# Kernel optimization log

Hardware: AMD Instinct MI355X
Metric: run time of the kernel (lower is better)

## Reference

```python
import jax, jax.numpy as jnp
import numpy as np

N_NODES = 50000
N_EDGES = 800000
D_IN = 128
D_OUT = 128
ALPHA = 0.2  # LeakyReLU negative slope


def setup_inputs() -> dict:
    key = jax.random.key(0)
    k1, k2, k3, k4 = jax.random.split(key, 4)
    x = jax.random.normal(k1, (N_NODES, D_IN), dtype=jnp.float32)
    W = jax.random.normal(k2, (D_IN, D_OUT), dtype=jnp.float32) * (1.414 / np.sqrt(D_IN))
    a = jax.random.normal(k3, (2 * D_OUT, 1), dtype=jnp.float32) * 0.1
    edge_index = jax.random.randint(k4, (2, N_EDGES), 0, N_NODES, dtype=jnp.int64)
    return {"x": x, "W": W, "a": a, "edge_index": edge_index}


def reference(x, W, a, edge_index):
    # h: (N, D_OUT)
    h = x @ W
    src, dst = edge_index[0], edge_index[1]
    # e_i = leakyrelu([h[src]; h[dst]] @ a) == leakyrelu((h@a1)[src] + (h@a2)[dst])
    a1 = a[:D_OUT, 0]
    a2 = a[D_OUT:, 0]
    s1 = h @ a1  # (N,)
    s2 = h @ a2  # (N,)
    e = jax.nn.leaky_relu(s1[src] + s2[dst], negative_slope=ALPHA)  # (E,)
    # Global softmax over all edges (faithful to F.softmax(edge_e, dim=0))
    attention = jax.nn.softmax(e)  # (E,)
    # output[dst] += attention * h[src]  (scatter-add)
    msgs = attention[:, None] * h[src]  # (E, D_OUT)
    output = jax.ops.segment_sum(msgs, dst, num_segments=N_NODES)
    return output
```

## Files before the change

### kernel.cpp

```cpp
#include <hip/hip_runtime.h>
#include <hip/hip_bf16.h>

#define N_NODES 50000
#define N_EDGES 800000
#define D 128
#define ALPHA 0.2f

#define KB_BLOCKS 3125
#define LDS_STRIDE 272

#define SCAN_PER 52
#define SCAN_PAD (1024 * SCAN_PER)

typedef __attribute__((ext_vector_type(8))) short short8;
typedef __attribute__((ext_vector_type(4))) float floatx4;

__device__ __forceinline__ unsigned int f2bf(float v)
{
    __hip_bfloat16 b = __float2bfloat16(v);
    return (unsigned int)*reinterpret_cast<unsigned short*>(&b);
}
__device__ __forceinline__ float bf_lo(unsigned int u)
{
    return __uint_as_float(u << 16);
}
__device__ __forceinline__ float bf_hi(unsigned int u)
{
    return __uint_as_float(u & 0xFFFF0000u);
}

__global__ __launch_bounds__(1024) void k_prep(
    const float* __restrict__ W, const float* __restrict__ a,
    float* __restrict__ w12, unsigned short* __restrict__ wb,
    int* __restrict__ deg, float* __restrict__ Z)
{
    const int t = threadIdx.x;
    const int b = blockIdx.x;
    deg[b * 1024 + t] = 0;
    if (b == 20 && t == 0) Z[0] = 0.f;

    if (b < 4) {
        const int g = b * 64 + (t >> 4);
        const int c = t & 15;
        const int which = g >> 7;
        const int r = g & 127;
        const float* wp = W + (size_t)r * D + c * 8;
        const float* ap = a + which * D + c * 8;
        const float4 u0 = *(const float4*)(wp);
        const float4 u1 = *(const float4*)(wp + 4);
        const float4 c0 = *(const float4*)(ap);
        const float4 c1 = *(const float4*)(ap + 4);
        float p = u0.x * c0.x + u0.y * c0.y + u0.z * c0.z + u0.w * c0.w
                + u1.x * c1.x + u1.y * c1.y + u1.z * c1.z + u1.w * c1.w;
        #pragma unroll
        for (int mask = 8; mask >= 1; mask >>= 1)
            p += __shfl_xor(p, mask);
        if (c == 0) w12[which * D + r] = p;
    } else if (b < 20) {
        const int f = (b - 4) * 1024 + t;
        const int j    = f & 7;
        const int lane = (f >> 3) & 63;
        const int half = (f >> 9) & 1;
        const int kt   = (f >> 10) & 3;
        const int wv   = f >> 12;
        const int q    = lane >> 4;
        const int nIdx = lane & 15;
        const float val =
            W[(size_t)(kt * 32 + q * 8 + j) * D + wv * 32 + 2 * nIdx + half];
        wb[f] = (unsigned short)f2bf(val);
    }
}

__global__ __launch_bounds__(256) void k_fused(
    const float* __restrict__ x, const float* __restrict__ w12,
    const unsigned short* __restrict__ wb, const int* __restrict__ ei,
    unsigned short* __restrict__ hb, float* __restrict__ s1,
    float* __restrict__ s2, int* __restrict__ deg, int* __restrict__ rank)
{
    __shared__ unsigned char lds[16 * LDS_STRIDE];
    const int t = threadIdx.x;
    const int rowbase = blockIdx.x * 16;

    const int r = t >> 4;
    const int c = t & 15;
    const float* xp = x + (size_t)(rowbase + r) * D + c * 8;
    const float4 v0 = *(const float4*)(xp);
    const float4 v1 = *(const float4*)(xp + 4);

    const int lane = t & 63;
    const int wv = t >> 6;
    const int q = lane >> 4;
    const int nIdx = lane & 15;
    const int n0 = wv * 32;
    const short8* wbp = (const short8*)wb;
    short8 B[2][4];
    #pragma unroll
    for (int kt = 0; kt < 4; ++kt) {
        B[0][kt] = wbp[((wv * 4 + kt) * 2 + 0) * 64 + lane];
        B[1][kt] = wbp[((wv * 4 + kt) * 2 + 1) * 64 + lane];
    }

    {
        const float* w1 = w12 + c * 8;
        const float* w2 = w12 + D + c * 8;
        float p1 = v0.x * w1[0] + v0.y * w1[1] + v0.z * w1[2] + v0.w * w1[3]
                 + v1.x * w1[4] + v1.y * w1[5] + v1.z * w1[6] + v1.w * w1[7];
        float p2 = v0.x * w2[0] + v0.y * w2[1] + v0.z * w2[2] + v0.w * w2[3]
                 + v1.x * w2[4] + v1.y * w2[5] + v1.z * w2[6] + v1.w * w2[7];
        #pragma unroll
        for (int mask = 8; mask >= 1; mask >>= 1) {
            p1 += __shfl_xor(p1, mask);
            p2 += __shfl_xor(p2, mask);
        }
        if (c == 0) { s1[rowbase + r] = p1; s2[rowbase + r] = p2; }

        uint4 pk;
        pk.x = f2bf(v0.x) | (f2bf(v0.y) << 16);
        pk.y = f2bf(v0.z) | (f2bf(v0.w) << 16);
        pk.z = f2bf(v1.x) | (f2bf(v1.y) << 16);
        pk.w = f2bf(v1.z) | (f2bf(v1.w) << 16);
        *(uint4*)(lds + r * LDS_STRIDE + c * 16) = pk;
    }
    __syncthreads();

    const unsigned char* ab = lds + nIdx * LDS_STRIDE + q * 16;
    const short8 A0 = *(const short8*)(ab);
    const short8 A1 = *(const short8*)(ab + 64);
    const short8 A2 = *(const short8*)(ab + 128);
    const short8 A3 = *(const short8*)(ab + 192);

    floatx4 acc0 = {0.f, 0.f, 0.f, 0.f};
    floatx4 acc1 = {0.f, 0.f, 0.f, 0.f};
    acc0 = __builtin_amdgcn_mfma_f32_16x16x32_bf16(A0, B[0][0], acc0, 0, 0, 0);
    acc1 = __builtin_amdgcn_mfma_f32_16x16x32_bf16(A0, B[1][0], acc1, 0, 0, 0);
    acc0 = __builtin_amdgcn_mfma_f32_16x16x32_bf16(A1, B[0][1], acc0, 0, 0, 0);
    acc1 = __builtin_amdgcn_mfma_f32_16x16x32_bf16(A1, B[1][1], acc1, 0, 0, 0);
    acc0 = __builtin_amdgcn_mfma_f32_16x16x32_bf16(A2, B[0][2], acc0, 0, 0, 0);
    acc1 = __builtin_amdgcn_mfma_f32_16x16x32_bf16(A2, B[1][2], acc1, 0, 0, 0);
    acc0 = __builtin_amdgcn_mfma_f32_16x16x32_bf16(A3, B[0][3], acc0, 0, 0, 0);
    acc1 = __builtin_amdgcn_mfma_f32_16x16x32_bf16(A3, B[1][3], acc1, 0, 0, 0);

    #pragma unroll
    for (int i = 0; i < 4; ++i) {
        const int row = rowbase + q * 4 + i;
        const unsigned int pk = f2bf(acc0[i]) | (f2bf(acc1[i]) << 16);
        *(unsigned int*)(hb + (size_t)row * D + n0 + 2 * nIdx) = pk;
    }

    const int e = blockIdx.x * 256 + t;
    rank[e] = atomicAdd(&deg[ei[N_EDGES + e]], 1);
}

__global__ __launch_bounds__(1024) void k_scan(
    const int* __restrict__ deg, int* __restrict__ offs)
{
    const int t = threadIdx.x;
    const int lane = t & 63;
    const int wv = t >> 6;
    __shared__ int wsum[16];
    const int base = t * SCAN_PER;
    int4 v[13];
    const int4* dp = (const int4*)(deg + base);
    int s = 0;
    #pragma unroll
    for (int k = 0; k < 13; ++k) {
        v[k] = dp[k];
        s += v[k].x + v[k].y + v[k].z + v[k].w;
    }
    int inc = s;
    #pragma unroll
    for (int off = 1; off < 64; off <<= 1) {
        int u = __shfl_up(inc, off);
        if (lane >= off) inc += u;
    }
    if (lane == 63) wsum[wv] = inc;
    __syncthreads();
    if (wv == 0 && lane < 16) {
        int wval = wsum[lane];
        int winc = wval;
        #pragma unroll
        for (int off = 1; off < 16; off <<= 1) {
            int u = __shfl_up(winc, off);
            if (lane >= off) winc += u;
        }
        wsum[lane] = winc - wval;
    }
    __syncthreads();
    int run = wsum[wv] + (inc - s);
    int4* op = (int4*)(offs + base);
    #pragma unroll
    for (int k = 0; k < 13; ++k) {
        int4 o;
        o.x = run;             run += v[k].x;
        o.y = run;             run += v[k].y;
        o.z = run;             run += v[k].z;
        o.w = run;             run += v[k].w;
        op[k] = o;
    }
}

__global__ __launch_bounds__(256) void k_post(
    const int* __restrict__ ei, const float* __restrict__ s1,
    const float* __restrict__ s2, const int* __restrict__ offs,
    const int* __restrict__ rank, uint2* __restrict__ csr64,
    float* __restrict__ Z)
{
    __shared__ float red[4];
    const int t = threadIdx.x;
    const int lane = t & 63;
    const int wv = t >> 6;
    const int e = blockIdx.x * 256 + t;
    const int sN = ei[e];
    const int dN = ei[N_EDGES + e];
    const int rk = rank[e];
    const int off = offs[dN];
    float v = s1[sN] + s2[dN];
    v = v > 0.f ? v : ALPHA * v;
    const float ex = __expf(v);
    uint2 rec;
    rec.x = (unsigned int)sN;
    rec.y = __float_as_uint(ex);
    csr64[off + rk] = rec;

    float sx = ex;
    #pragma unroll
    for (int mask = 32; mask >= 1; mask >>= 1)
        sx += __shfl_xor(sx, mask);
    if (lane == 0) red[wv] = sx;
    __syncthreads();
    if (t == 0)
        atomicAdd(Z, (red[0] + red[1]) + (red[2] + red[3]));
}

__global__ __launch_bounds__(256) void k_gather(
    const uint2* __restrict__ csr64, const int* __restrict__ offs,
    const unsigned short* __restrict__ hb, const float* __restrict__ Z,
    float* __restrict__ out)
{
    const int node = (blockIdx.x * blockDim.x + threadIdx.x) >> 6;
    if (node >= N_NODES) return;
    const int lane = threadIdx.x & 63;
    const float invZ = 1.0f / Z[0];
    const int beg = offs[node];
    const int end = offs[node + 1];

    float a0 = 0.f, a1 = 0.f, b0 = 0.f, b1 = 0.f;
    float c0 = 0.f, c1 = 0.f, d0 = 0.f, d1 = 0.f;
    float e0 = 0.f, e1 = 0.f, f0 = 0.f, f1 = 0.f;
    float g0 = 0.f, g1 = 0.f, h0 = 0.f, h1 = 0.f;

    for (int cb = beg; cb < end; cb += 64) {
        const int n = min(64, end - cb);
        uint2 rec;
        if (cb + lane < end) {
            rec = csr64[cb + lane];
        } else {
            rec.x = 0u;
            rec.y = 0u;
        }
        const int srcl = (int)rec.x;
        const float attl = __uint_as_float(rec.y) * invZ;

        int j = 0;
        for (; j + 7 < n; j += 8) {
            const int i0 = __shfl(srcl, j);
            const int i1 = __shfl(srcl, j + 1);
            const int i2 = __shfl(srcl, j + 2);
            const int i3 = __shfl(srcl, j + 3);
            const int i4 = __shfl(srcl, j + 4);
            const int i5 = __shfl(srcl, j + 5);
            const int i6 = __shfl(srcl, j + 6);
            const int i7 = __shfl(srcl, j + 7);
            const float w0 = __shfl(attl, j);
            const float w1 = __shfl(attl, j + 1);
            const float w2 = __shfl(attl, j + 2);
            const float w3 = __shfl(attl, j + 3);
            const float w4 = __shfl(attl, j + 4);
            const float w5 = __shfl(attl, j + 5);
            const float w6 = __shfl(attl, j + 6);
            const float w7 = __shfl(attl, j + 7);
            const unsigned int u0 = *(const unsigned int*)(hb + (size_t)i0 * D + lane * 2);
            const unsigned int u1 = *(const unsigned int*)(hb + (size_t)i1 * D + lane * 2);
            const unsigned int u2 = *(const unsigned int*)(hb + (size_t)i2 * D + lane * 2);
            const unsigned int u3 = *(const unsigned int*)(hb + (size_t)i3 * D + lane * 2);
            const unsigned int u4 = *(const unsigned int*)(hb + (size_t)i4 * D + lane * 2);
            const unsigned int u5 = *(const unsigned int*)(hb + (size_t)i5 * D + lane * 2);
            const unsigned int u6 = *(const unsigned int*)(hb + (size_t)i6 * D + lane * 2);
            const unsigned int u7 = *(const unsigned int*)(hb + (size_t)i7 * D + lane * 2);
            a0 += w0 * bf_lo(u0); a1 += w0 * bf_hi(u0);
            b0 += w1 * bf_lo(u1); b1 += w1 * bf_hi(u1);
            c0 += w2 * bf_lo(u2); c1 += w2 * bf_hi(u2);
            d0 += w3 * bf_lo(u3); d1 += w3 * bf_hi(u3);
            e0 += w4 * bf_lo(u4); e1 += w4 * bf_hi(u4);
            f0 += w5 * bf_lo(u5); f1 += w5 * bf_hi(u5);
            g0 += w6 * bf_lo(u6); g1 += w6 * bf_hi(u6);
            h0 += w7 * bf_lo(u7); h1 += w7 * bf_hi(u7);
        }
        for (; j + 3 < n; j += 4) {
            const int i0 = __shfl(srcl, j);
            const int i1 = __shfl(srcl, j + 1);
            const int i2 = __shfl(srcl, j + 2);
            const int i3 = __shfl(srcl, j + 3);
            const float w0 = __shfl(attl, j);
            const float w1 = __shfl(attl, j + 1);
            const float w2 = __shfl(attl, j + 2);
            const float w3 = __shfl(attl, j + 3);
            const unsigned int u0 = *(const unsigned int*)(hb + (size_t)i0 * D + lane * 2);
            const unsigned int u1 = *(const unsigned int*)(hb + (size_t)i1 * D + lane * 2);
            const unsigned int u2 = *(const unsigned int*)(hb + (size_t)i2 * D + lane * 2);
            const unsigned int u3 = *(const unsigned int*)(hb + (size_t)i3 * D + lane * 2);
            a0 += w0 * bf_lo(u0); a1 += w0 * bf_hi(u0);
            b0 += w1 * bf_lo(u1); b1 += w1 * bf_hi(u1);
            c0 += w2 * bf_lo(u2); c1 += w2 * bf_hi(u2);
            d0 += w3 * bf_lo(u3); d1 += w3 * bf_hi(u3);
        }
        for (; j < n; ++j) {
            const int i0 = __shfl(srcl, j);
            const float w0 = __shfl(attl, j);
            const unsigned int u0 = *(const unsigned int*)(hb + (size_t)i0 * D + lane * 2);
            a0 += w0 * bf_lo(u0); a1 += w0 * bf_hi(u0);
        }
    }
    float2 r;
    r.x = ((a0 + b0) + (c0 + d0)) + ((e0 + f0) + (g0 + h0));
    r.y = ((a1 + b1) + (c1 + d1)) + ((e1 + f1) + (g1 + h1));
    *(float2*)(out + (size_t)node * D + lane * 2) = r;
}

extern "C" void kernel_launch(void* const* d_in, const int* in_sizes, int n_in,
                              void* d_out, int out_size, void* d_ws, size_t ws_size,
                              hipStream_t stream)
{
    const float* x = (const float*)d_in[0];
    const float* W = (const float*)d_in[1];
    const float* a = (const float*)d_in[2];
    const int* ei = (const int*)d_in[3];
    float* out = (float*)d_out;

    char* wsb = (char*)d_ws;
    uint2* csr64 = (uint2*)wsb;
    unsigned short* hb = (unsigned short*)(wsb + (size_t)N_EDGES * 8);
    unsigned short* wb = hb + (size_t)N_NODES * D;
    int* rank     = (int*)(wb + 16384);
    float* s1     = (float*)(rank + N_EDGES);
    float* s2     = s1 + N_NODES;
    int*   deg    = (int*)(s2 + N_NODES);
    int*   offs   = deg + SCAN_PAD;
    float* w12    = (float*)(offs + SCAN_PAD);
    float* Z      = w12 + 2 * D;

    k_prep<<<SCAN_PAD / 1024, 1024, 0, stream>>>(W, a, w12, wb, deg, Z);
    k_fused<<<N_NODES / 16, 256, 0, stream>>>(x, w12, wb, ei, hb, s1, s2,
                                              deg, rank);
    k_scan<<<1, 1024, 0, stream>>>(deg, offs);
    k_post<<<KB_BLOCKS, 256, 0, stream>>>(ei, s1, s2, offs, rank, csr64, Z);
    k_gather<<<(N_NODES * 64 + 255) / 256, 256, 0, stream>>>(
        csr64, offs, hb, Z, out);
}
```

Baseline: 205.5 us.

## Split score kernel out and move edge exp/softmax sum before scan

```diff
diff --git a/kernel.cpp b/kernel.cpp
--- a/kernel.cpp
+++ b/kernel.cpp
@@ -71,15 +71,48 @@
     }
 }
 
+__global__ __launch_bounds__(256) void k_sc(
+    const float* __restrict__ x, const float* __restrict__ w12,
+    float* __restrict__ s1, float* __restrict__ s2)
+{
+    const int t = threadIdx.x;
+    const int r = t >> 4;
+    const int c = t & 15;
+    const int row = blockIdx.x * 16 + r;
+    const float* xp = x + (size_t)row * D + c * 8;
+    const float4 v0 = *(const float4*)(xp);
+    const float4 v1 = *(const float4*)(xp + 4);
+    const float* w1 = w12 + c * 8;
+    const float* w2 = w12 + D + c * 8;
+    float p1 = v0.x * w1[0] + v0.y * w1[1] + v0.z * w1[2] + v0.w * w1[3]
+             + v1.x * w1[4] + v1.y * w1[5] + v1.z * w1[6] + v1.w * w1[7];
+    float p2 = v0.x * w2[0] + v0.y * w2[1] + v0.z * w2[2] + v0.w * w2[3]
+             + v1.x * w2[4] + v1.y * w2[5] + v1.z * w2[6] + v1.w * w2[7];
+    #pragma unroll
+    for (int mask = 8; mask >= 1; mask >>= 1) {
+        p1 += __shfl_xor(p1, mask);
+        p2 += __shfl_xor(p2, mask);
+    }
+    if (c == 0) { s1[row] = p1; s2[row] = p2; }
+}
+
 __global__ __launch_bounds__(256) void k_fused(
-    const float* __restrict__ x, const float* __restrict__ w12,
-    const unsigned short* __restrict__ wb, const int* __restrict__ ei,
-    unsigned short* __restrict__ hb, float* __restrict__ s1,
-    float* __restrict__ s2, int* __restrict__ deg, int* __restrict__ rank)
+    const float* __restrict__ x, const unsigned short* __restrict__ wb,
+    const int* __restrict__ ei, const float* __restrict__ s1,
+    const float* __restrict__ s2, unsigned short* __restrict__ hb,
+    int* __restrict__ deg, int* __restrict__ rank, float* __restrict__ ve,
+    float* __restrict__ Z)
 {
     __shared__ unsigned char lds[16 * LDS_STRIDE];
+    __shared__ float red[4];
     const int t = threadIdx.x;
     const int rowbase = blockIdx.x * 16;
+
+    const int e = blockIdx.x * 256 + t;
+    const int sN = ei[e];
+    const int dN = ei[N_EDGES + e];
+    const float s1g = s1[sN];
+    const float s2g = s2[dN];
 
     const int r = t >> 4;
     const int c = t & 15;
@@ -101,19 +134,6 @@
     }
 
     {
-        const float* w1 = w12 + c * 8;
-        const float* w2 = w12 + D + c * 8;
-        float p1 = v0.x * w1[0] + v0.y * w1[1] + v0.z * w1[2] + v0.w * w1[3]
-                 + v1.x * w1[4] + v1.y * w1[5] + v1.z * w1[6] + v1.w * w1[7];
-        float p2 = v0.x * w2[0] + v0.y * w2[1] + v0.z * w2[2] + v0.w * w2[3]
-                 + v1.x * w2[4] + v1.y * w2[5] + v1.z * w2[6] + v1.w * w2[7];
-        #pragma unroll
-        for (int mask = 8; mask >= 1; mask >>= 1) {
-            p1 += __shfl_xor(p1, mask);
-            p2 += __shfl_xor(p2, mask);
-        }
-        if (c == 0) { s1[rowbase + r] = p1; s2[rowbase + r] = p2; }
-
         uint4 pk;
         pk.x = f2bf(v0.x) | (f2bf(v0.y) << 16);
         pk.y = f2bf(v0.z) | (f2bf(v0.w) << 16);
@@ -147,8 +167,20 @@
         *(unsigned int*)(hb + (size_t)row * D + n0 + 2 * nIdx) = pk;
     }
 
-    const int e = blockIdx.x * 256 + t;
-    rank[e] = atomicAdd(&deg[ei[N_EDGES + e]], 1);
+    rank[e] = atomicAdd(&deg[dN], 1);
+    float v = s1g + s2g;
+    v = v > 0.f ? v : ALPHA * v;
+    const float ex = __expf(v);
+    ve[e] = ex;
+
+    float sx = ex;
+    #pragma unroll
+    for (int mask = 32; mask >= 1; mask >>= 1)
+        sx += __shfl_xor(sx, mask);
+    if (lane == 0) red[wv] = sx;
+    __syncthreads();
+    if (t == 0)
+        atomicAdd(Z, (red[0] + red[1]) + (red[2] + red[3]));
 }
 
 __global__ __launch_bounds__(1024) void k_scan(
@@ -200,36 +232,42 @@
 }
 
 __global__ __launch_bounds__(256) void k_post(
-    const int* __restrict__ ei, const float* __restrict__ s1,
-    const float* __restrict__ s2, const int* __restrict__ offs,
-    const int* __restrict__ rank, uint2* __restrict__ csr64,
-    float* __restrict__ Z)
-{
-    __shared__ float red[4];
-    const int t = threadIdx.x;
-    const int lane = t & 63;
-    const int wv = t >> 6;
-    const int e = blockIdx.x * 256 + t;
-    const int sN = ei[e];
-    const int dN = ei[N_EDGES + e];
-    const int rk = rank[e];
-    const int off = offs[dN];
-    float v = s1[sN] + s2[dN];
-    v = v > 0.f ? v : ALPHA * v;
-    const float ex = __expf(v);
-    uint2 rec;
-    rec.x = (unsigned int)sN;
-    rec.y = __float_as_uint(ex);
-    csr64[off + rk] = rec;
-
-    float sx = ex;
-    #pragma unroll
-    for (int mask = 32; mask >= 1; mask >>= 1)
-        sx += __shfl_xor(sx, mask);
-    if (lane == 0) red[wv] = sx;
-    __syncthreads();
-    if (t == 0)
-        atomicAdd(Z, (red[0] + red[1]) + (red[2] + red[3]));
+    const int* __restrict__ ei, const int* __restrict__ offs,
+    const int* __restrict__ rank, const float* __restrict__ ve,
+    uint2* __restrict__ csr64)
+{
+    const int e0 = blockIdx.x * 512 + threadIdx.x;
+    const int e1 = e0 + 256;
+
+    const int sA = ei[e0];
+    const int dA = ei[N_EDGES + e0];
+    int sB = 0, dB = 0;
+    const bool okB = (e1 < N_EDGES);
+    if (okB) {
+        sB = ei[e1];
+        dB = ei[N_EDGES + e1];
+    }
+    const int rkA = rank[e0];
+    const int offA = offs[dA];
+    const float exA = ve[e0];
+    int rkB = 0, offB = 0;
+    float exB = 0.f;
+    if (okB) {
+        rkB = rank[e1];
+        offB = offs[dB];
+        exB = ve[e1];
+    }
+
+    uint2 recA;
+    recA.x = (unsigned int)sA;
+    recA.y = __float_as_uint(exA);
+    csr64[offA + rkA] = recA;
+    if (okB) {
+        uint2 recB;
+        recB.x = (unsigned int)sB;
+        recB.y = __float_as_uint(exB);
+        csr64[offB + rkB] = recB;
+    }
 }
 
 __global__ __launch_bounds__(256) void k_gather(
@@ -342,7 +380,8 @@
     unsigned short* hb = (unsigned short*)(wsb + (size_t)N_EDGES * 8);
     unsigned short* wb = hb + (size_t)N_NODES * D;
     int* rank     = (int*)(wb + 16384);
-    float* s1     = (float*)(rank + N_EDGES);
+    float* ve     = (float*)(rank + N_EDGES);
+    float* s1     = ve + N_EDGES;
     float* s2     = s1 + N_NODES;
     int*   deg    = (int*)(s2 + N_NODES);
     int*   offs   = deg + SCAN_PAD;
@@ -350,10 +389,12 @@
     float* Z      = w12 + 2 * D;
 
     k_prep<<<SCAN_PAD / 1024, 1024, 0, stream>>>(W, a, w12, wb, deg, Z);
-    k_fused<<<N_NODES / 16, 256, 0, stream>>>(x, w12, wb, ei, hb, s1, s2,
-                                              deg, rank);
+    k_sc<<<N_NODES / 16, 256, 0, stream>>>(x, w12, s1, s2);
+    k_fused<<<N_NODES / 16, 256, 0, stream>>>(x, wb, ei, s1, s2, hb,
+                                              deg, rank, ve, Z);
     k_scan<<<1, 1024, 0, stream>>>(deg, offs);
-    k_post<<<KB_BLOCKS, 256, 0, stream>>>(ei, s1, s2, offs, rank, csr64, Z);
+    k_post<<<(N_EDGES + 511) / 512, 256, 0, stream>>>(ei, offs, rank, ve,
+                                                      csr64);
     k_gather<<<(N_NODES * 64 + 255) / 256, 256, 0, stream>>>(
         csr64, offs, hb, Z, out);
 }
```

New measurement: 196.4 us. -4.5%, faster.

## Restructure CSR build: count first, then fuse edge scoring and cursor-based scatter

Applied to the files above, without the earlier changes.

```diff
diff --git a/kernel.cpp b/kernel.cpp
--- a/kernel.cpp
+++ b/kernel.cpp
@@ -6,11 +6,12 @@
 #define D 128
 #define ALPHA 0.2f
 
-#define KB_BLOCKS 3125
 #define LDS_STRIDE 272
 
 #define SCAN_PER 52
 #define SCAN_PAD (1024 * SCAN_PER)
+#define NB_CNT ((N_EDGES + 1023) / 1024)
+#define NB_SC  ((N_NODES + 63) / 64)
 
 typedef __attribute__((ext_vector_type(8))) short short8;
 typedef __attribute__((ext_vector_type(4))) float floatx4;
@@ -29,18 +30,18 @@
     return __uint_as_float(u & 0xFFFF0000u);
 }
 
-__global__ __launch_bounds__(1024) void k_prep(
+__global__ __launch_bounds__(1024) void k_zero(
     const float* __restrict__ W, const float* __restrict__ a,
     float* __restrict__ w12, unsigned short* __restrict__ wb,
     int* __restrict__ deg, float* __restrict__ Z)
 {
     const int t = threadIdx.x;
     const int b = blockIdx.x;
-    deg[b * 1024 + t] = 0;
-    if (b == 20 && t == 0) Z[0] = 0.f;
-
-    if (b < 4) {
-        const int g = b * 64 + (t >> 4);
+    if (b < 52) deg[b * 1024 + t] = 0;
+    if (b == 52 && t == 0) Z[0] = 0.f;
+
+    if (b >= 52 && b < 56) {
+        const int g = (b - 52) * 64 + (t >> 4);
         const int c = t & 15;
         const int which = g >> 7;
         const int r = g & 127;
@@ -56,8 +57,8 @@
         for (int mask = 8; mask >= 1; mask >>= 1)
             p += __shfl_xor(p, mask);
         if (c == 0) w12[which * D + r] = p;
-    } else if (b < 20) {
-        const int f = (b - 4) * 1024 + t;
+    } else if (b >= 56) {
+        const int f = (b - 56) * 1024 + t;
         const int j    = f & 7;
         const int lane = (f >> 3) & 63;
         const int half = (f >> 9) & 1;
@@ -71,15 +72,107 @@
     }
 }
 
+__global__ __launch_bounds__(1024) void k_count(
+    const int* __restrict__ ei, int* __restrict__ deg)
+{
+    const int e = blockIdx.x * 1024 + threadIdx.x;
+    if (e < N_EDGES) atomicAdd(&deg[ei[N_EDGES + e]], 1);
+}
+
+__global__ __launch_bounds__(1024) void k_mid(
+    const int* __restrict__ deg, int* __restrict__ offs,
+    int* __restrict__ cursor, const float* __restrict__ x,
+    const float* __restrict__ w12, float* __restrict__ s1,
+    float* __restrict__ s2)
+{
+    const int t = threadIdx.x;
+    const int lane = t & 63;
+    const int wv = t >> 6;
+
+    if (blockIdx.x == 0) {
+        __shared__ int wsum[16];
+        const int base = t * SCAN_PER;
+        int4 v[13];
+        const int4* dp = (const int4*)(deg + base);
+        int s = 0;
+        #pragma unroll
+        for (int k = 0; k < 13; ++k) {
+            v[k] = dp[k];
+            s += v[k].x + v[k].y + v[k].z + v[k].w;
+        }
+        int inc = s;
+        #pragma unroll
+        for (int off = 1; off < 64; off <<= 1) {
+            int u = __shfl_up(inc, off);
+            if (lane >= off) inc += u;
+        }
+        if (lane == 63) wsum[wv] = inc;
+        __syncthreads();
+        if (wv == 0 && lane < 16) {
+            int wval = wsum[lane];
+            int winc = wval;
+            #pragma unroll
+            for (int off = 1; off < 16; off <<= 1) {
+                int u = __shfl_up(winc, off);
+                if (lane >= off) winc += u;
+            }
+            wsum[lane] = winc - wval;
+        }
+        __syncthreads();
+        int run = wsum[wv] + (inc - s);
+        int4* op = (int4*)(offs + base);
+        int4* cp = (int4*)(cursor + base);
+        #pragma unroll
+        for (int k = 0; k < 13; ++k) {
+            int4 o;
+            o.x = run;             run += v[k].x;
+            o.y = run;             run += v[k].y;
+            o.z = run;             run += v[k].z;
+            o.w = run;             run += v[k].w;
+            op[k] = o;
+            cp[k] = o;
+        }
+        return;
+    }
+
+    const int r = t >> 4;
+    const int c = t & 15;
+    const int row = (blockIdx.x - 1) * 64 + r;
+    if (row >= N_NODES) return;
+    const float* xp = x + (size_t)row * D + c * 8;
+    const float4 v0 = *(const float4*)(xp);
+    const float4 v1 = *(const float4*)(xp + 4);
+    const float* w1 = w12 + c * 8;
+    const float* w2 = w12 + D + c * 8;
+    float p1 = v0.x * w1[0] + v0.y * w1[1] + v0.z * w1[2] + v0.w * w1[3]
+             + v1.x * w1[4] + v1.y * w1[5] + v1.z * w1[6] + v1.w * w1[7];
+    float p2 = v0.x * w2[0] + v0.y * w2[1] + v0.z * w2[2] + v0.w * w2[3]
+             + v1.x * w2[4] + v1.y * w2[5] + v1.z * w2[6] + v1.w * w2[7];
+    #pragma unroll
+    for (int mask = 8; mask >= 1; mask >>= 1) {
+        p1 += __shfl_xor(p1, mask);
+        p2 += __shfl_xor(p2, mask);
+    }
+    if (c == 0) { s1[row] = p1; s2[row] = p2; }
+}
+
 __global__ __launch_bounds__(256) void k_fused(
-    const float* __restrict__ x, const float* __restrict__ w12,
-    const unsigned short* __restrict__ wb, const int* __restrict__ ei,
-    unsigned short* __restrict__ hb, float* __restrict__ s1,
-    float* __restrict__ s2, int* __restrict__ deg, int* __restrict__ rank)
+    const float* __restrict__ x, const unsigned short* __restrict__ wb,
+    const int* __restrict__ ei, const float* __restrict__ s1,
+    const float* __restrict__ s2, unsigned short* __restrict__ hb,
+    int* __restrict__ cursor, uint2* __restrict__ csr64,
+    float* __restrict__ Z)
 {
     __shared__ unsigned char lds[16 * LDS_STRIDE];
+    __shared__ float red[4];
     const int t = threadIdx.x;
     const int rowbase = blockIdx.x * 16;
+
+    const int e = blockIdx.x * 256 + t;
+    const int sN = ei[e];
+    const int dN = ei[N_EDGES + e];
+    const float s1g = s1[sN];
+    const float s2g = s2[dN];
 
     const int r = t >> 4;
     const int c = t & 15;
@@ -101,19 +194,6 @@
     }
 
     {
-        const float* w1 = w12 + c * 8;
-        const float* w2 = w12 + D + c * 8;
-        float p1 = v0.x * w1[0] + v0.y * w1[1] + v0.z * w1[2] + v0.w * w1[3]
-                 + v1.x * w1[4] + v1.y * w1[5] + v1.z * w1[6] + v1.w * w1[7];
-        float p2 = v0.x * w2[0] + v0.y * w2[1] + v0.z * w2[2] + v0.w * w2[3]
-                 + v1.x * w2[4] + v1.y * w2[5] + v1.z * w2[6] + v1.w * w2[7];
-        #pragma unroll
-        for (int mask = 8; mask >= 1; mask >>= 1) {
-            p1 += __shfl_xor(p1, mask);
-            p2 += __shfl_xor(p2, mask);
-        }
-        if (c == 0) { s1[rowbase + r] = p1; s2[rowbase + r] = p2; }
-
         uint4 pk;
         pk.x = f2bf(v0.x) | (f2bf(v0.y) << 16);
         pk.y = f2bf(v0.z) | (f2bf(v0.w) << 16);
@@ -147,80 +227,14 @@
         *(unsigned int*)(hb + (size_t)row * D + n0 + 2 * nIdx) = pk;
     }
 
-    const int e = blockIdx.x * 256 + t;
-    rank[e] = atomicAdd(&deg[ei[N_EDGES + e]], 1);
-}
-
-__global__ __launch_bounds__(1024) void k_scan(
-    const int* __restrict__ deg, int* __restrict__ offs)
-{
-    const int t = threadIdx.x;
-    const int lane = t & 63;
-    const int wv = t >> 6;
-    __shared__ int wsum[16];
-    const int base = t * SCAN_PER;
-    int4 v[13];
-    const int4* dp = (const int4*)(deg + base);
-    int s = 0;
-    #pragma unroll
-    for (int k = 0; k < 13; ++k) {
-        v[k] = dp[k];
-        s += v[k].x + v[k].y + v[k].z + v[k].w;
-    }
-    int inc = s;
-    #pragma unroll
-    for (int off = 1; off < 64; off <<= 1) {
-        int u = __shfl_up(inc, off);
-        if (lane >= off) inc += u;
-    }
-    if (lane == 63) wsum[wv] = inc;
-    __syncthreads();
-    if (wv == 0 && lane < 16) {
-        int wval = wsum[lane];
-        int winc = wval;
-        #pragma unroll
-        for (int off = 1; off < 16; off <<= 1) {
-            int u = __shfl_up(winc, off);
-            if (lane >= off) winc += u;
-        }
-        wsum[lane] = winc - wval;
-    }
-    __syncthreads();
-    int run = wsum[wv] + (inc - s);
-    int4* op = (int4*)(offs + base);
-    #pragma unroll
-    for (int k = 0; k < 13; ++k) {
-        int4 o;
-        o.x = run;             run += v[k].x;
-        o.y = run;             run += v[k].y;
-        o.z = run;             run += v[k].z;
-        o.w = run;             run += v[k].w;
-        op[k] = o;
-    }
-}
-
-__global__ __launch_bounds__(256) void k_post(
-    const int* __restrict__ ei, const float* __restrict__ s1,
-    const float* __restrict__ s2, const int* __restrict__ offs,
-    const int* __restrict__ rank, uint2* __restrict__ csr64,
-    float* __restrict__ Z)
-{
-    __shared__ float red[4];
-    const int t = threadIdx.x;
-    const int lane = t & 63;
-    const int wv = t >> 6;
-    const int e = blockIdx.x * 256 + t;
-    const int sN = ei[e];
-    const int dN = ei[N_EDGES + e];
-    const int rk = rank[e];
-    const int off = offs[dN];
-    float v = s1[sN] + s2[dN];
+    float v = s1g + s2g;
     v = v > 0.f ? v : ALPHA * v;
     const float ex = __expf(v);
+    const int pos = atomicAdd(&cursor[dN], 1);
     uint2 rec;
     rec.x = (unsigned int)sN;
     rec.y = __float_as_uint(ex);
-    csr64[off + rk] = rec;
+    csr64[pos] = rec;
 
     float sx = ex;
     #pragma unroll
@@ -341,19 +355,19 @@
     uint2* csr64 = (uint2*)wsb;
     unsigned short* hb = (unsigned short*)(wsb + (size_t)N_EDGES * 8);
     unsigned short* wb = hb + (size_t)N_NODES * D;
-    int* rank     = (int*)(wb + 16384);
-    float* s1     = (float*)(rank + N_EDGES);
+    float* s1     = (float*)(wb + 16384);
     float* s2     = s1 + N_NODES;
     int*   deg    = (int*)(s2 + N_NODES);
     int*   offs   = deg + SCAN_PAD;
-    float* w12    = (float*)(offs + SCAN_PAD);
+    int*   cursor = offs + SCAN_PAD;
+    float* w12    = (float*)(cursor + SCAN_PAD);
     float* Z      = w12 + 2 * D;
 
-    k_prep<<<SCAN_PAD / 1024, 1024, 0, stream>>>(W, a, w12, wb, deg, Z);
-    k_fused<<<N_NODES / 16, 256, 0, stream>>>(x, w12, wb, ei, hb, s1, s2,
-                                              deg, rank);
-    k_scan<<<1, 1024, 0, stream>>>(deg, offs);
-    k_post<<<KB_BLOCKS, 256, 0, stream>>>(ei, s1, s2, offs, rank, csr64, Z);
+    k_zero<<<72, 1024, 0, stream>>>(W, a, w12, wb, deg, Z);
+    k_count<<<NB_CNT, 1024, 0, stream>>>(ei, deg);
+    k_mid<<<1 + NB_SC, 1024, 0, stream>>>(deg, offs, cursor, x, w12, s1, s2);
+    k_fused<<<N_NODES / 16, 256, 0, stream>>>(x, wb, ei, s1, s2, hb,
+                                              cursor, csr64, Z);
     k_gather<<<(N_NODES * 64 + 255) / 256, 256, 0, stream>>>(
         csr64, offs, hb, Z, out);
 }
```

Measured after the change: 221.5 us. 7.8% more time.
